# Optimization experiments

Measured on AMD Instinct MI355X. Metric: run time of the kernel, lower is better.

## Reference

```python
import jax, jax.numpy as jnp
import numpy as np

N_NODES = 50000
N_EDGES = 1_600_000
IN_DIM = 6
EMB = 64
EDGE_DIM = 1
L = 4
BN_EPS = 1e-5


def _bn_relu(x, gamma, beta):
    # BatchNorm1d in training mode: biased batch stats over the row dim.
    mu = jnp.mean(x, axis=0)
    var = jnp.var(x, axis=0)
    xhat = (x - mu) * jax.lax.rsqrt(var + BN_EPS)
    return jax.nn.relu(xhat * gamma + beta)


def setup_inputs() -> dict:
    key = jax.random.key(0)
    ks = jax.random.split(key, 32)
    s = 0.1
    inp = {
        "x": jax.random.normal(ks[0], (N_NODES, IN_DIM), jnp.float32),
        "edge_index": jax.random.randint(ks[1], (2, N_EDGES), 0, N_NODES),
        "edge_attr": jax.random.normal(ks[2], (N_EDGES, EDGE_DIM), jnp.float32),
        "lin_in_W": jax.random.normal(ks[3], (IN_DIM, EMB)) * s,
        "lin_in_b": jnp.zeros((EMB,)),
        # per-layer stacked params, leading dim L
        "msg_W1": jax.random.normal(ks[4], (L, 2 * EMB + EDGE_DIM, EMB)) * s,
        "msg_b1": jnp.zeros((L, EMB)),
        "msg_g1": jnp.ones((L, EMB)),
        "msg_be1": jnp.zeros((L, EMB)),
        "msg_W2": jax.random.normal(ks[5], (L, EMB, EMB)) * s,
        "msg_b2": jnp.zeros((L, EMB)),
        "msg_g2": jnp.ones((L, EMB)),
        "msg_be2": jnp.zeros((L, EMB)),
        "upd_W1": jax.random.normal(ks[6], (L, 2 * EMB, EMB)) * s,
        "upd_b1": jnp.zeros((L, EMB)),
        "upd_g1": jnp.ones((L, EMB)),
        "upd_be1": jnp.zeros((L, EMB)),
        "upd_W2": jax.random.normal(ks[7], (L, EMB, EMB)) * s,
        "upd_b2": jnp.zeros((L, EMB)),
        "upd_g2": jnp.ones((L, EMB)),
        "upd_be2": jnp.zeros((L, EMB)),
        "pred_W": jax.random.normal(ks[8], (EMB, 1)) * s,
        "pred_b": jnp.zeros((1,)),
    }
    return inp


def reference(x, edge_index, edge_attr, lin_in_W, lin_in_b,
              msg_W1, msg_b1, msg_g1, msg_be1, msg_W2, msg_b2, msg_g2, msg_be2,
              upd_W1, upd_b1, upd_g1, upd_be1, upd_W2, upd_b2, upd_g2, upd_be2,
              pred_W, pred_b):
    n = x.shape[0]
    src = edge_index[0]  # j (source)
    dst = edge_index[1]  # i (target / aggregation index)

    h = x @ lin_in_W + lin_in_b  # (n, d)
    for l in range(L):
        h_i = h[dst]                              # (e, d) destination feats
        h_j = h[src]                              # (e, d) source feats
        m = jnp.concatenate([h_i, h_j, edge_attr], axis=-1)  # (e, 2d+de)
        m = _bn_relu(m @ msg_W1[l] + msg_b1[l], msg_g1[l], msg_be1[l])
        m = _bn_relu(m @ msg_W2[l] + msg_b2[l], msg_g2[l], msg_be2[l])
        aggr = jax.ops.segment_sum(m, dst, num_segments=n)   # (n, d)
        u = jnp.concatenate([h, aggr], axis=-1)              # (n, 2d)
        u = _bn_relu(u @ upd_W1[l] + upd_b1[l], upd_g1[l], upd_be1[l])
        u = _bn_relu(u @ upd_W2[l] + upd_b2[l], upd_g2[l], upd_be2[l])
        h = h + u  # residual
    out = h @ pred_W + pred_b
    return out.reshape(-1)
```

## Files before the change

### kernel.cpp

```cpp
#include <hip/hip_runtime.h>
#include <hip/hip_bf16.h>


#define BN_EPS 1e-5f
#define NSH 128
#define LYS 72
#define LW1S 168
#define LW2S 68
#define ASW 66

typedef __attribute__((ext_vector_type(8))) short short8;
typedef __attribute__((ext_vector_type(16))) float floatx16;

#define MFMA32 __builtin_amdgcn_mfma_f32_32x32x16_bf16

__device__ __forceinline__ short f2bs(float f) {
  union { float f; unsigned u; } x; x.f = f;
  unsigned r = x.u + 0x7fffu + ((x.u >> 16) & 1u);
  return (short)(r >> 16);
}
__device__ __forceinline__ short f2bs_fast(float f) {
  union { float f; unsigned u; } x; x.f = f;
  return (short)((x.u + 0x8000u) >> 16);
}
__device__ __forceinline__ float bs2f(short s) {
  union { unsigned u; float f; } x;
  x.u = ((unsigned)(unsigned short)s) << 16;
  return x.f;
}


__global__ void lin_in_kernel(const float* __restrict__ x,
                              const float* __restrict__ W,
                              const float* __restrict__ b, float* __restrict__ h,
                              short* __restrict__ hb, int N) {
  int gid = blockIdx.x * blockDim.x + threadIdx.x;
  if (gid >= N * 64) return;
  int n = gid >> 6, o = gid & 63;
  float acc = b[o];
#pragma unroll
  for (int k = 0; k < 6; ++k) acc += x[n * 6 + k] * W[k * 64 + o];
  h[gid] = acc;
  hb[gid] = f2bs(acc);
}

__global__ void deg_kernel(const int* __restrict__ ei, int* __restrict__ deg,
                           int E) {
  int gid = blockIdx.x * blockDim.x + threadIdx.x;
  if (gid < E) atomicAdd(&deg[ei[E + gid]], 1);
}

__global__ void scan_kernel(const int* __restrict__ deg, int* __restrict__ offs,
                            int N) {
  __shared__ int s[1024];
  int t = threadIdx.x;
  int chunk = (N + 1023) >> 10;
  int lo = t * chunk, hi = lo + chunk;
  if (hi > N) hi = N;
  if (lo > N) lo = N;
  int tot = 0;
  for (int i = lo; i < hi; ++i) tot += deg[i];
  s[t] = tot;
  __syncthreads();
  for (int off = 1; off < 1024; off <<= 1) {
    int v = (t >= off) ? s[t - off] : 0;
    __syncthreads();
    s[t] += v;
    __syncthreads();
  }
  int run = s[t] - tot;
  for (int i = lo; i < hi; ++i) {
    offs[i] = run;
    run += deg[i];
  }
}

__global__ void fill_kernel(const int* __restrict__ ei,
                            const int* __restrict__ offs, int* __restrict__ cnt,
                            int* __restrict__ sorted, int E) {
  int gid = blockIdx.x * blockDim.x + threadIdx.x;
  if (gid >= E) return;
  int d = ei[E + gid];
  int pos = offs[d] + atomicAdd(&cnt[d], 1);
  sorted[pos] = gid;
}

__global__ void gather_edges_kernel(const int* __restrict__ ei,
                                    const int* __restrict__ sorted,
                                    const float* __restrict__ ea,
                                    int* __restrict__ dd, int* __restrict__ ds,
                                    short* __restrict__ es, int E, int Epad) {
  int i = blockIdx.x * 256 + threadIdx.x;
  if (i >= Epad) return;
  if (i < E) {
    int e = sorted[i];
    dd[i] = ei[E + e];
    ds[i] = ei[e];
    es[i] = f2bs(ea[e]);
  } else {
    dd[i] = -1;
    ds[i] = 0;
    es[i] = 0;
  }
}

__global__ void pack_w1_kernel(const float* __restrict__ W,
                               short* __restrict__ Wt, int L_) {
  int i = blockIdx.x * 256 + threadIdx.x;
  if (i >= L_ * 64 * 160) return;
  int k = i % 160, n = (i / 160) % 64, l = i / (160 * 64);
  Wt[i] = (k < 129) ? f2bs(W[((size_t)l * 129 + k) * 64 + n]) : (short)0;
}

__global__ void pack_w2_kernel(const float* __restrict__ W,
                               short* __restrict__ Wt, int L_) {
  int i = blockIdx.x * 256 + threadIdx.x;
  if (i >= L_ * 64 * 64) return;
  int k = i % 64, n = (i / 64) % 64, l = i / 4096;
  Wt[i] = f2bs(W[((size_t)l * 64 + k) * 64 + n]);
}

__global__ void bn_finalize_kernel(const float* __restrict__ shards,
                                   const float* __restrict__ gamma,
                                   const float* __restrict__ beta, float cnt,
                                   float* __restrict__ ac) {
  int o = threadIdx.x;
  float s = 0.f, q = 0.f;
  for (int i = 0; i < NSH; ++i) {
    s += shards[i * 128 + o];
    q += shards[i * 128 + 64 + o];
  }
  float mu = s / cnt;
  float var = fmaxf(q / cnt - mu * mu, 0.f);
  float r = rsqrtf(var + BN_EPS);
  float g = gamma[o];
  ac[o] = g * r;
  ac[64 + o] = beta[o] - mu * g * r;
}

__global__ void bn_finalize_pack1(const float* __restrict__ shards,
                                  const float* __restrict__ gamma,
                                  const float* __restrict__ beta, float cnt,
                                  const float* __restrict__ W,
                                  const float* __restrict__ b,
                                  short* __restrict__ Wt,
                                  float* __restrict__ bs) {
  __shared__ float sa[64];
  int t = threadIdx.x;
  if (t < 64) {
    float s = 0.f, q = 0.f;
    for (int i = 0; i < NSH; ++i) {
      s += shards[i * 128 + t];
      q += shards[i * 128 + 64 + t];
    }
    float mu = s / cnt;
    float var = fmaxf(q / cnt - mu * mu, 0.f);
    float r = rsqrtf(var + BN_EPS);
    float a = gamma[t] * r;
    float c = beta[t] - mu * a;
    sa[t] = a;
    if (blockIdx.x == 0) bs[t] = a * b[t] + c;
  }
  __syncthreads();
  int i = blockIdx.x * 256 + t;
  if (i < 64 * 160) {
    int k = i % 160, n = i / 160;
    Wt[i] = (k < 129) ? f2bs(W[k * 64 + n] * sa[n]) : (short)0;
  }
}

__global__ void bn_finalize_pack2(const float* __restrict__ shards,
                                  const float* __restrict__ gamma,
                                  const float* __restrict__ beta, float cnt,
                                  const float* __restrict__ W,
                                  const float* __restrict__ b,
                                  short* __restrict__ Wt,
                                  float* __restrict__ bs) {
  __shared__ float sa[64];
  int t = threadIdx.x;
  if (t < 64) {
    float s = 0.f, q = 0.f;
    for (int i = 0; i < NSH; ++i) {
      s += shards[i * 128 + t];
      q += shards[i * 128 + 64 + t];
    }
    float mu = s / cnt;
    float var = fmaxf(q / cnt - mu * mu, 0.f);
    float r = rsqrtf(var + BN_EPS);
    float a = gamma[t] * r;
    float c = beta[t] - mu * a;
    sa[t] = a;
    if (blockIdx.x == 0) bs[t] = a * b[t] + c;
  }
  __syncthreads();
  int i = blockIdx.x * 256 + t;
  if (i < 64 * 64) {
    int k = i % 64, n = i / 64;
    Wt[i] = f2bs(W[k * 64 + n] * sa[n]);
  }
}


__device__ __forceinline__ void stage_w1(const short* __restrict__ Wt,
                                         short* Lw, int t) {
#pragma unroll
  for (int i = 0; i < 5; ++i) {
    int c = t + i * 256;
    int col = c / 20, ch = c % 20;
    *(short8*)&Lw[col * LW1S + ch * 8] = *(const short8*)&Wt[col * 160 + ch * 8];
  }
}
__device__ __forceinline__ void stage_w2(const short* __restrict__ Wt,
                                         short* Lw, int t) {
#pragma unroll
  for (int i = 0; i < 2; ++i) {
    int c = t + i * 256;
    int col = c >> 3, ch = c & 7;
    *(short8*)&Lw[col * LW2S + ch * 8] = *(const short8*)&Wt[col * 64 + ch * 8];
  }
}

__device__ __forceinline__ void gemm1_32(const short* __restrict__ hbf,
                                         const short* Lw1,
                                         const float* __restrict__ bias, int d,
                                         int sx, short eav, int me, int hl,
                                         floatx16 acc[2]) {
  const short* hd = hbf + (size_t)d * 64 + hl * 8;
  const short* hs = hbf + (size_t)sx * 64 + hl * 8;
  short8 A[8];
#pragma unroll
  for (int kc = 0; kc < 4; ++kc) A[kc] = *(const short8*)(hd + kc * 16);
#pragma unroll
  for (int kc = 0; kc < 4; ++kc) A[4 + kc] = *(const short8*)(hs + kc * 16);
  short8 a8 = {0, 0, 0, 0, 0, 0, 0, 0};
  if (hl == 0) a8[0] = eav;
#pragma unroll
  for (int nt = 0; nt < 2; ++nt) {
    int col = nt * 32 + me;
    float bv = bias[col];
    floatx16 a;
#pragma unroll
    for (int r = 0; r < 16; ++r) a[r] = bv;
    const short* wp = Lw1 + col * LW1S + hl * 8;
#pragma unroll
    for (int kc = 0; kc < 8; ++kc) {
      short8 B = *(const short8*)(wp + kc * 16);
      a = MFMA32(A[kc], B, a, 0, 0, 0);
    }
    short8 B8 = *(const short8*)(wp + 128);
    a = MFMA32(a8, B8, a, 0, 0, 0);
    acc[nt] = a;
  }
}

__device__ __forceinline__ void gemm2_32(const short* Ly, const short* Lw2,
                                         const float* __restrict__ bias, int w,
                                         int me, int hl, floatx16 acc[2]) {
  short8 Z[4];
  const short* zp = &Ly[(w * 32 + me) * LYS + hl * 8];
#pragma unroll
  for (int kc = 0; kc < 4; ++kc) Z[kc] = *(const short8*)(zp + kc * 16);
#pragma unroll
  for (int nt = 0; nt < 2; ++nt) {
    int col = nt * 32 + me;
    float bv = bias[col];
    floatx16 a;
#pragma unroll
    for (int r = 0; r < 16; ++r) a[r] = bv;
    const short* wp = Lw2 + col * LW2S + hl * 8;
#pragma unroll
    for (int kc = 0; kc < 4; ++kc) {
      short8 B = *(const short8*)(wp + kc * 16);
      a = MFMA32(Z[kc], B, a, 0, 0, 0);
    }
    acc[nt] = a;
  }
}

__device__ __forceinline__ void stats32(const floatx16 acc[2], int idx0, int w,
                                        int hl, int lane, int E, bool full,
                                        float* sredw) {
#pragma unroll
  for (int nt = 0; nt < 2; ++nt) {
    float s = 0.f, q = 0.f;
#pragma unroll
    for (int r = 0; r < 16; ++r) {
      float v = acc[nt][r];
      if (!full) {
        int row = (r & 3) + 8 * (r >> 2) + 4 * hl;
        if (idx0 + w * 32 + row >= E) v = 0.f;
      }
      s += v;
      q += v * v;
    }
    s += __shfl_down(s, 32, 64);
    q += __shfl_down(q, 32, 64);
    if (lane < 32) {
      sredw[nt * 32 + lane] = s;
      sredw[64 + nt * 32 + lane] = q;
    }
  }
}

__device__ __forceinline__ void write_ly(short* Ly, const floatx16 acc[2],
                                         int w, int me, int hl, bool mask,
                                         int idx0, int E) {
#pragma unroll
  for (int nt = 0; nt < 2; ++nt) {
    int col = nt * 32 + me;
#pragma unroll
    for (int r = 0; r < 16; ++r) {
      int row = (r & 3) + 8 * (r >> 2) + 4 * hl;
      float v = fmaxf(acc[nt][r], 0.f);
      if (mask && idx0 + w * 32 + row >= E) v = 0.f;
      Ly[(w * 32 + row) * LYS + col] = f2bs_fast(v);
    }
  }
}


__global__ __launch_bounds__(256) void edge_pass_a(
    const short* __restrict__ hbf, const short* __restrict__ Wt1,
    const float* __restrict__ b1, const int* __restrict__ dd,
    const int* __restrict__ dsr, const short* __restrict__ es,
    float* __restrict__ stat, int E) {
  __shared__ __align__(16) short Lw1[64 * LW1S];
  __shared__ float sred[4][128];
  int t = threadIdx.x, idx0 = blockIdx.x * 128;
  stage_w1(Wt1, Lw1, t);
  __syncthreads();
  int w = t >> 6, lane = t & 63, me = lane & 31, hl = lane >> 5;
  int eg = idx0 + w * 32 + me;
  int d = dd[eg];
  int dc = d < 0 ? 0 : d;
  int sx = dsr[eg];
  short eav = es[eg];
  floatx16 acc[2];
  gemm1_32(hbf, Lw1, b1, dc, sx, eav, me, hl, acc);
  bool full = idx0 + 128 <= E;
  stats32(acc, idx0, w, hl, lane, E, full, sred[w]);
  __syncthreads();
  if (t < 128) {
    float v = sred[0][t] + sred[1][t] + sred[2][t] + sred[3][t];
    atomicAdd(&stat[(size_t)(blockIdx.x & (NSH - 1)) * 128 + t], v);
  }
}

__global__ __launch_bounds__(256) void edge_pass_b(
    const short* __restrict__ hbf, const short* __restrict__ Wt1s,
    const float* __restrict__ b1s, const int* __restrict__ dd,
    const int* __restrict__ dsr, const short* __restrict__ es,
    const short* __restrict__ Wt2, const float* __restrict__ b2,
    float* __restrict__ stat, int E) {
  __shared__ __align__(16) short Lw1[64 * LW1S];
  __shared__ __align__(16) short Lw2[64 * LW2S];
  __shared__ __align__(16) short Ly[128 * LYS];
  __shared__ float sred[4][128];
  int t = threadIdx.x, idx0 = blockIdx.x * 128;
  stage_w1(Wt1s, Lw1, t);
  stage_w2(Wt2, Lw2, t);
  __syncthreads();
  int w = t >> 6, lane = t & 63, me = lane & 31, hl = lane >> 5;
  int eg = idx0 + w * 32 + me;
  int d = dd[eg];
  int dc = d < 0 ? 0 : d;
  int sx = dsr[eg];
  short eav = es[eg];
  floatx16 acc[2];
  gemm1_32(hbf, Lw1, b1s, dc, sx, eav, me, hl, acc);
  write_ly(Ly, acc, w, me, hl, false, idx0, E);
  floatx16 acc2[2];
  gemm2_32(Ly, Lw2, b2, w, me, hl, acc2);
  bool full = idx0 + 128 <= E;
  stats32(acc2, idx0, w, hl, lane, E, full, sred[w]);
  __syncthreads();
  if (t < 128) {
    float v = sred[0][t] + sred[1][t] + sred[2][t] + sred[3][t];
    atomicAdd(&stat[(size_t)(blockIdx.x & (NSH - 1)) * 128 + t], v);
  }
}

__global__ __launch_bounds__(256) void edge_pass_c(
    const short* __restrict__ hbf, const short* __restrict__ Wt1s,
    const float* __restrict__ b1s, const int* __restrict__ dd,
    const int* __restrict__ dsr, const short* __restrict__ es,
    const short* __restrict__ Wt2s, const float* __restrict__ b2s,
    float* __restrict__ aggr, int E) {
  __shared__ __align__(16) short Lw1[64 * LW1S];
  __shared__ __align__(16) short Lw2[64 * LW2S];
  __shared__ __align__(16) short Ly[128 * LYS];
  __shared__ int sdst[128];
  int t = threadIdx.x, idx0 = blockIdx.x * 128;
  if (t < 128) sdst[t] = dd[idx0 + t];
  stage_w1(Wt1s, Lw1, t);
  stage_w2(Wt2s, Lw2, t);
  __syncthreads();
  int w = t >> 6, lane = t & 63, me = lane & 31, hl = lane >> 5;
  int eg = idx0 + w * 32 + me;
  int d = sdst[w * 32 + me];
  int dc = d < 0 ? 0 : d;
  int sx = dsr[eg];
  short eav = es[eg];
  floatx16 acc[2];
  gemm1_32(hbf, Lw1, b1s, dc, sx, eav, me, hl, acc);
  write_ly(Ly, acc, w, me, hl, false, idx0, E);
  floatx16 acc2[2];
  gemm2_32(Ly, Lw2, b2s, w, me, hl, acc2);
  bool full = idx0 + 128 <= E;
  write_ly(Ly, acc2, w, me, hl, !full, idx0, E);
  __syncthreads();
  int scol = t & 63, g = t >> 6;
  float s = 0.f;
  int e0 = g * 32;
  for (int e = e0; e < e0 + 32; ++e) {
    int d2 = sdst[e];
    s += bs2f(Ly[e * LYS + scol]);
    int dn = (e == e0 + 31) ? -2 : sdst[e + 1];
    if (d2 != dn) {
      if (d2 >= 0) atomicAdd(&aggr[(size_t)d2 * 64 + scol], s);
      s = 0.f;
    }
  }
}


__device__ __forceinline__ void gemm_r2c8(const float* __restrict__ As,
                                          const float* __restrict__ W, int K,
                                          int rg, int cg, float acc[2][8]) {
  const float* ap = As + rg * 2;
  const float* wp = W + cg * 8;
#pragma unroll 4
  for (int k = 0; k < K; ++k) {
    float2 a = *(const float2*)&ap[k * ASW];
    float4 w0 = *(const float4*)&wp[k * 64];
    float4 w1 = *(const float4*)&wp[k * 64 + 4];
    float wv[8] = {w0.x, w0.y, w0.z, w0.w, w1.x, w1.y, w1.z, w1.w};
#pragma unroll
    for (int j = 0; j < 8; ++j) {
      acc[0][j] += a.x * wv[j];
      acc[1][j] += a.y * wv[j];
    }
  }
}

__device__ __forceinline__ void stats_r2c8(const float acc[2][8],
                                           float* __restrict__ shard, int t,
                                           int cg) {
  float s[8], q[8];
#pragma unroll
  for (int j = 0; j < 8; ++j) {
    s[j] = acc[0][j] + acc[1][j];
    q[j] = acc[0][j] * acc[0][j] + acc[1][j] * acc[1][j];
  }
#pragma unroll
  for (int off = 32; off >= 8; off >>= 1) {
#pragma unroll
    for (int j = 0; j < 8; ++j) {
      s[j] += __shfl_down(s[j], off, 64);
      q[j] += __shfl_down(q[j], off, 64);
    }
  }
  if (((t & 63) >> 3) == 0) {
#pragma unroll
    for (int j = 0; j < 8; ++j) {
      atomicAdd(&shard[cg * 8 + j], s[j]);
      atomicAdd(&shard[64 + cg * 8 + j], q[j]);
    }
  }
}

__global__ __launch_bounds__(256) void node_gemm1_v3(
    const float* __restrict__ h, const float* __restrict__ aggr,
    const float* __restrict__ W, const float* __restrict__ b,
    float* __restrict__ u1, float* __restrict__ stat, int N) {
  __shared__ __align__(16) float As[128 * ASW];
  int n0 = blockIdx.x * 64;
  int t = threadIdx.x;
  int c = t & 63, g = t >> 6;
  for (int n = g; n < 64; n += 4) {
    int idx = n0 + n;
    bool v = idx < N;
    As[c * ASW + n] = v ? h[(size_t)idx * 64 + c] : 0.f;
    As[(64 + c) * ASW + n] = v ? aggr[(size_t)idx * 64 + c] : 0.f;
  }
  __syncthreads();
  int rg = t >> 3, cg = t & 7;
  float acc[2][8];
#pragma unroll
  for (int i = 0; i < 2; ++i)
#pragma unroll
    for (int j = 0; j < 8; ++j) acc[i][j] = b[cg * 8 + j];
  gemm_r2c8(As, W, 128, rg, cg, acc);
#pragma unroll
  for (int i = 0; i < 2; ++i) {
    int idx = n0 + rg * 2 + i;
    if (idx < N) {
      *(float4*)&u1[(size_t)idx * 64 + cg * 8] =
          make_float4(acc[i][0], acc[i][1], acc[i][2], acc[i][3]);
      *(float4*)&u1[(size_t)idx * 64 + cg * 8 + 4] =
          make_float4(acc[i][4], acc[i][5], acc[i][6], acc[i][7]);
    } else {
#pragma unroll
      for (int j = 0; j < 8; ++j) acc[i][j] = 0.f;
    }
  }
  stats_r2c8(acc, stat + (size_t)(blockIdx.x & (NSH - 1)) * 128, t, cg);
}

__global__ __launch_bounds__(256) void node_gemm2_v3(
    const float* __restrict__ u1, const float* __restrict__ ac,
    const float* __restrict__ W, const float* __restrict__ b,
    float* __restrict__ u2, float* __restrict__ stat, int N) {
  __shared__ __align__(16) float As[64 * ASW];
  int n0 = blockIdx.x * 64;
  int t = threadIdx.x;
  int c = t & 63, g = t >> 6;
  float a1 = ac[c], c1 = ac[64 + c];
  for (int n = g; n < 64; n += 4) {
    int idx = n0 + n;
    bool v = idx < N;
    As[c * ASW + n] = v ? fmaxf(u1[(size_t)idx * 64 + c] * a1 + c1, 0.f) : 0.f;
  }
  __syncthreads();
  int rg = t >> 3, cg = t & 7;
  float acc[2][8];
#pragma unroll
  for (int i = 0; i < 2; ++i)
#pragma unroll
    for (int j = 0; j < 8; ++j) acc[i][j] = b[cg * 8 + j];
  gemm_r2c8(As, W, 64, rg, cg, acc);
#pragma unroll
  for (int i = 0; i < 2; ++i) {
    int idx = n0 + rg * 2 + i;
    if (idx < N) {
      *(float4*)&u2[(size_t)idx * 64 + cg * 8] =
          make_float4(acc[i][0], acc[i][1], acc[i][2], acc[i][3]);
      *(float4*)&u2[(size_t)idx * 64 + cg * 8 + 4] =
          make_float4(acc[i][4], acc[i][5], acc[i][6], acc[i][7]);
    } else {
#pragma unroll
      for (int j = 0; j < 8; ++j) acc[i][j] = 0.f;
    }
  }
  stats_r2c8(acc, stat + (size_t)(blockIdx.x & (NSH - 1)) * 128, t, cg);
}

__global__ void residual_kernel(float* __restrict__ h, short* __restrict__ hb,
                                const float* __restrict__ u2,
                                const float* __restrict__ ac, int total) {
  int gid = blockIdx.x * blockDim.x + threadIdx.x;
  if (gid >= total) return;
  int o = gid & 63;
  float v = u2[gid] * ac[o] + ac[64 + o];
  float nv = h[gid] + fmaxf(v, 0.f);
  h[gid] = nv;
  hb[gid] = f2bs(nv);
}

__global__ void pred_kernel(const float* __restrict__ h,
                            const float* __restrict__ W,
                            const float* __restrict__ b,
                            float* __restrict__ out, int N) {
  int n = blockIdx.x * blockDim.x + threadIdx.x;
  if (n >= N) return;
  float acc = b[0];
  const float* hr = h + (size_t)n * 64;
#pragma unroll
  for (int o = 0; o < 64; ++o) acc += hr[o] * W[o];
  out[n] = acc;
}


extern "C" void kernel_launch(void* const* d_in, const int* in_sizes, int n_in,
                              void* d_out, int out_size, void* d_ws,
                              size_t ws_size, hipStream_t stream) {
  const float* x = (const float*)d_in[0];
  const int* ei = (const int*)d_in[1];
  const float* ea = (const float*)d_in[2];
  const float* lin_W = (const float*)d_in[3];
  const float* lin_b = (const float*)d_in[4];
  const float* msg_W1 = (const float*)d_in[5];
  const float* msg_b1 = (const float*)d_in[6];
  const float* msg_g1 = (const float*)d_in[7];
  const float* msg_be1 = (const float*)d_in[8];
  const float* msg_W2 = (const float*)d_in[9];
  const float* msg_b2 = (const float*)d_in[10];
  const float* msg_g2 = (const float*)d_in[11];
  const float* msg_be2 = (const float*)d_in[12];
  const float* upd_W1 = (const float*)d_in[13];
  const float* upd_b1 = (const float*)d_in[14];
  const float* upd_g1 = (const float*)d_in[15];
  const float* upd_be1 = (const float*)d_in[16];
  const float* upd_W2 = (const float*)d_in[17];
  const float* upd_b2 = (const float*)d_in[18];
  const float* upd_g2 = (const float*)d_in[19];
  const float* upd_be2 = (const float*)d_in[20];
  const float* pred_W = (const float*)d_in[21];
  const float* pred_b = (const float*)d_in[22];
  float* out = (float*)d_out;

  const int N = in_sizes[0] / 6;
  const int E = in_sizes[1] / 2;
  const int L = 4;
  const int Epad = ((E + 127) / 128) * 128;

  char* p = (char*)d_ws;
  auto alloc = [&](size_t bytes) {
    void* r = (void*)p;
    p += (bytes + 255) & ~(size_t)255;
    return r;
  };
  float* h = (float*)alloc((size_t)N * 64 * 4);
  short* hb = (short*)alloc((size_t)N * 64 * 2);
  float* aggr = (float*)alloc((size_t)N * 64 * 4);
  float* u1 = (float*)alloc((size_t)N * 64 * 4);
  float* u2 = (float*)alloc((size_t)N * 64 * 4);
  float* stats = (float*)alloc((size_t)4 * NSH * 128 * 4);
  float* acu1 = (float*)alloc(128 * 4);
  float* acu2 = (float*)alloc(128 * 4);
  float* b1s = (float*)alloc(64 * 4);
  float* b2s = (float*)alloc(64 * 4);
  int* deg = (int*)alloc((size_t)N * 4);
  int* offs = (int*)alloc((size_t)N * 4);
  int* cnt = (int*)alloc((size_t)N * 4);
  int* sorted = (int*)alloc((size_t)E * 4);
  int* dd = (int*)alloc((size_t)Epad * 4);
  int* dsr = (int*)alloc((size_t)Epad * 4);
  short* es = (short*)alloc((size_t)Epad * 2);
  short* Wt1 = (short*)alloc((size_t)L * 64 * 160 * 2);
  short* Wt2 = (short*)alloc((size_t)L * 64 * 64 * 2);
  short* Wt1s = (short*)alloc((size_t)64 * 160 * 2);
  short* Wt2s = (short*)alloc((size_t)64 * 64 * 2);

  const int B = 256;
  const size_t REG = (size_t)NSH * 128;
  int gridE256 = (E + 255) / 256;
  int gridEb = Epad / 128;
  int gridM64 = (N + 63) / 64;
  int gridN64 = (N * 64 + B - 1) / B;
  int gridN = (N + B - 1) / B;

  hipMemsetAsync(deg, 0, (size_t)N * 4, stream);
  hipMemsetAsync(cnt, 0, (size_t)N * 4, stream);
  lin_in_kernel<<<gridN64, B, 0, stream>>>(x, lin_W, lin_b, h, hb, N);
  deg_kernel<<<gridE256, B, 0, stream>>>(ei, deg, E);
  scan_kernel<<<1, 1024, 0, stream>>>(deg, offs, N);
  fill_kernel<<<gridE256, B, 0, stream>>>(ei, offs, cnt, sorted, E);
  gather_edges_kernel<<<(Epad + 255) / 256, B, 0, stream>>>(ei, sorted, ea, dd,
                                                            dsr, es, E, Epad);
  pack_w1_kernel<<<(L * 64 * 160 + 255) / 256, B, 0, stream>>>(msg_W1, Wt1, L);
  pack_w2_kernel<<<(L * 64 * 64 + 255) / 256, B, 0, stream>>>(msg_W2, Wt2, L);

  for (int l = 0; l < L; ++l) {
    const short* Wt1l = Wt1 + (size_t)l * 64 * 160;
    const short* Wt2l = Wt2 + (size_t)l * 64 * 64;
    const float* U1 = upd_W1 + (size_t)l * 128 * 64;
    const float* U2 = upd_W2 + (size_t)l * 64 * 64;
    hipMemsetAsync(stats, 0, (size_t)4 * REG * 4, stream);
    hipMemsetAsync(aggr, 0, (size_t)N * 64 * 4, stream);
    edge_pass_a<<<gridEb, 256, 0, stream>>>(hb, Wt1l, msg_b1 + l * 64, dd, dsr,
                                            es, stats, E);
    bn_finalize_pack1<<<(64 * 160 + 255) / 256, B, 0, stream>>>(
        stats, msg_g1 + l * 64, msg_be1 + l * 64, (float)E,
        msg_W1 + (size_t)l * 129 * 64, msg_b1 + l * 64, Wt1s, b1s);
    edge_pass_b<<<gridEb, 256, 0, stream>>>(hb, Wt1s, b1s, dd, dsr, es, Wt2l,
                                            msg_b2 + l * 64, stats + REG, E);
    bn_finalize_pack2<<<(64 * 64 + 255) / 256, B, 0, stream>>>(
        stats + REG, msg_g2 + l * 64, msg_be2 + l * 64, (float)E,
        msg_W2 + (size_t)l * 64 * 64, msg_b2 + l * 64, Wt2s, b2s);
    edge_pass_c<<<gridEb, 256, 0, stream>>>(hb, Wt1s, b1s, dd, dsr, es, Wt2s,
                                            b2s, aggr, E);
    node_gemm1_v3<<<gridM64, 256, 0, stream>>>(h, aggr, U1, upd_b1 + l * 64,
                                               u1, stats + 2 * REG, N);
    bn_finalize_kernel<<<1, 64, 0, stream>>>(stats + 2 * REG, upd_g1 + l * 64,
                                             upd_be1 + l * 64, (float)N, acu1);
    node_gemm2_v3<<<gridM64, 256, 0, stream>>>(u1, acu1, U2, upd_b2 + l * 64,
                                               u2, stats + 3 * REG, N);
    bn_finalize_kernel<<<1, 64, 0, stream>>>(stats + 3 * REG, upd_g2 + l * 64,
                                             upd_be2 + l * 64, (float)N, acu2);
    residual_kernel<<<gridN64, B, 0, stream>>>(h, hb, u2, acu2, N * 64);
  }
  pred_kernel<<<gridN, B, 0, stream>>>(h, pred_W, pred_b, out, N);
}
```

Measured before the change: 2.082 ms.

## Cache pre-BN edge activations in workspace instead of recomputing edge GEMMs

Pass A now writes the raw first-layer message GEMM output to a bf16 workspace buffer, and pass B reads it back, applies the BN affine and ReLU, and runs only the second GEMM. Pass B also stores its raw output so pass C only needs the BN affine, ReLU and segment-sum, with no GEMMs. This removes the recomputed gathers and MFMA work in passes B and C. In exchange it adds large global reads and writes, and edges beyond the workspace capacity fall back to recomputation. It also loops several tiles per block, stores node intermediates u1/u2 as bf16, and merges the two memsets into one.

New measurement: 2.420 ms. 1.16x slower.

```diff
diff --git a/kernel.cpp b/kernel.cpp
--- a/kernel.cpp
+++ b/kernel.cpp
@@ -4,6 +4,7 @@
 
 #define BN_EPS 1e-5f
 #define NSH 128
+#define TPB 4
 #define LYS 72
 #define LW1S 168
 #define LW2S 68
@@ -143,8 +144,8 @@
                                   const float* __restrict__ beta, float cnt,
                                   const float* __restrict__ W,
                                   const float* __restrict__ b,
-                                  short* __restrict__ Wt,
-                                  float* __restrict__ bs) {
+                                  short* __restrict__ Wt, float* __restrict__ bs,
+                                  float* __restrict__ ac) {
   __shared__ float sa[64];
   int t = threadIdx.x;
   if (t < 64) {
@@ -159,7 +160,11 @@
     float a = gamma[t] * r;
     float c = beta[t] - mu * a;
     sa[t] = a;
-    if (blockIdx.x == 0) bs[t] = a * b[t] + c;
+    if (blockIdx.x == 0) {
+      bs[t] = a * b[t] + c;
+      ac[t] = a;
+      ac[64 + t] = c;
+    }
   }
   __syncthreads();
   int i = blockIdx.x * 256 + t;
@@ -174,8 +179,8 @@
                                   const float* __restrict__ beta, float cnt,
                                   const float* __restrict__ W,
                                   const float* __restrict__ b,
-                                  short* __restrict__ Wt,
-                                  float* __restrict__ bs) {
+                                  short* __restrict__ Wt, float* __restrict__ bs,
+                                  float* __restrict__ ac) {
   __shared__ float sa[64];
   int t = threadIdx.x;
   if (t < 64) {
@@ -190,7 +195,11 @@
     float a = gamma[t] * r;
     float c = beta[t] - mu * a;
     sa[t] = a;
-    if (blockIdx.x == 0) bs[t] = a * b[t] + c;
+    if (blockIdx.x == 0) {
+      bs[t] = a * b[t] + c;
+      ac[t] = a;
+      ac[64 + t] = c;
+    }
   }
   __syncthreads();
   int i = blockIdx.x * 256 + t;
@@ -253,13 +262,16 @@
   }
 }
 
-__device__ __forceinline__ void gemm2_32(const short* Ly, const short* Lw2,
-                                         const float* __restrict__ bias, int w,
-                                         int me, int hl, floatx16 acc[2]) {
-  short8 Z[4];
+__device__ __forceinline__ void load_z_ly(const short* Ly, int w, int me,
+                                          int hl, short8 Z[4]) {
   const short* zp = &Ly[(w * 32 + me) * LYS + hl * 8];
 #pragma unroll
   for (int kc = 0; kc < 4; ++kc) Z[kc] = *(const short8*)(zp + kc * 16);
+}
+
+__device__ __forceinline__ void gemm2_core(const short8 Z[4], const short* Lw2,
+                                           const float* __restrict__ bias,
+                                           int me, int hl, floatx16 acc[2]) {
 #pragma unroll
   for (int nt = 0; nt < 2; ++nt) {
     int col = nt * 32 + me;
@@ -277,9 +289,9 @@
   }
 }
 
-__device__ __forceinline__ void stats32(const floatx16 acc[2], int idx0, int w,
-                                        int hl, int lane, int E, bool full,
-                                        float* sredw) {
+__device__ __forceinline__ void stats32_acc(const floatx16 acc[2], int idx0,
+                                            int w, int hl, int E, bool full,
+                                            float sa[2], float qa[2]) {
 #pragma unroll
   for (int nt = 0; nt < 2; ++nt) {
     float s = 0.f, q = 0.f;
@@ -295,10 +307,8 @@
     }
     s += __shfl_down(s, 32, 64);
     q += __shfl_down(q, 32, 64);
-    if (lane < 32) {
-      sredw[nt * 32 + lane] = s;
-      sredw[64 + nt * 32 + lane] = q;
-    }
+    sa[nt] += s;
+    qa[nt] += q;
   }
 }
 
@@ -318,27 +328,70 @@
   }
 }
 
+__device__ __forceinline__ void write_ly_raw(short* Ly, const floatx16 acc[2],
+                                             int w, int me, int hl) {
+#pragma unroll
+  for (int nt = 0; nt < 2; ++nt) {
+    int col = nt * 32 + me;
+#pragma unroll
+    for (int r = 0; r < 16; ++r) {
+      int row = (r & 3) + 8 * (r >> 2) + 4 * hl;
+      Ly[(w * 32 + row) * LYS + col] = f2bs_fast(acc[nt][r]);
+    }
+  }
+}
+
+__device__ __forceinline__ void ly_to_g(const short* Ly, short* y, int t) {
+#pragma unroll
+  for (int i = 0; i < 4; ++i) {
+    int c = t + i * 256;
+    int row = c >> 3, ch = c & 7;
+    *(short8*)&y[(size_t)row * 64 + ch * 8] =
+        *(const short8*)&Ly[row * LYS + ch * 8];
+  }
+}
+
 
 __global__ __launch_bounds__(256) void edge_pass_a(
     const short* __restrict__ hbf, const short* __restrict__ Wt1,
     const float* __restrict__ b1, const int* __restrict__ dd,
     const int* __restrict__ dsr, const short* __restrict__ es,
-    float* __restrict__ stat, int E) {
+    float* __restrict__ stat, short* __restrict__ ybuf, int E, int Epad,
+    int Ecap) {
   __shared__ __align__(16) short Lw1[64 * LW1S];
+  __shared__ __align__(16) short Ly[128 * LYS];
   __shared__ float sred[4][128];
-  int t = threadIdx.x, idx0 = blockIdx.x * 128;
+  int t = threadIdx.x;
   stage_w1(Wt1, Lw1, t);
   __syncthreads();
   int w = t >> 6, lane = t & 63, me = lane & 31, hl = lane >> 5;
-  int eg = idx0 + w * 32 + me;
-  int d = dd[eg];
-  int dc = d < 0 ? 0 : d;
-  int sx = dsr[eg];
-  short eav = es[eg];
-  floatx16 acc[2];
-  gemm1_32(hbf, Lw1, b1, dc, sx, eav, me, hl, acc);
-  bool full = idx0 + 128 <= E;
-  stats32(acc, idx0, w, hl, lane, E, full, sred[w]);
+  float sa[2] = {0.f, 0.f}, qa[2] = {0.f, 0.f};
+  for (int it = 0; it < TPB; ++it) {
+    int idx0 = (blockIdx.x * TPB + it) * 128;
+    if (idx0 >= Epad) break;
+    int eg = idx0 + w * 32 + me;
+    int d = dd[eg];
+    int dc = d < 0 ? 0 : d;
+    int sx = dsr[eg];
+    short eav = es[eg];
+    floatx16 acc[2];
+    gemm1_32(hbf, Lw1, b1, dc, sx, eav, me, hl, acc);
+    bool full = idx0 + 128 <= E;
+    stats32_acc(acc, idx0, w, hl, E, full, sa, qa);
+    if (idx0 < Ecap) {
+      write_ly_raw(Ly, acc, w, me, hl);
+      __syncthreads();
+      ly_to_g(Ly, ybuf + (size_t)idx0 * 64, t);
+      __syncthreads();
+    }
+  }
+  if (lane < 32) {
+#pragma unroll
+    for (int nt = 0; nt < 2; ++nt) {
+      sred[w][nt * 32 + lane] = sa[nt];
+      sred[w][64 + nt * 32 + lane] = qa[nt];
+    }
+  }
   __syncthreads();
   if (t < 128) {
     float v = sred[0][t] + sred[1][t] + sred[2][t] + sred[3][t];
@@ -348,31 +401,73 @@
 
 __global__ __launch_bounds__(256) void edge_pass_b(
     const short* __restrict__ hbf, const short* __restrict__ Wt1s,
-    const float* __restrict__ b1s, const int* __restrict__ dd,
-    const int* __restrict__ dsr, const short* __restrict__ es,
-    const short* __restrict__ Wt2, const float* __restrict__ b2,
-    float* __restrict__ stat, int E) {
+    const float* __restrict__ b1s, const float* __restrict__ ac1,
+    const int* __restrict__ dd, const int* __restrict__ dsr,
+    const short* __restrict__ es, const short* __restrict__ Wt2,
+    const float* __restrict__ b2, float* __restrict__ stat,
+    short* __restrict__ ybuf, int E, int Epad, int Ecap) {
   __shared__ __align__(16) short Lw1[64 * LW1S];
   __shared__ __align__(16) short Lw2[64 * LW2S];
   __shared__ __align__(16) short Ly[128 * LYS];
   __shared__ float sred[4][128];
-  int t = threadIdx.x, idx0 = blockIdx.x * 128;
-  stage_w1(Wt1s, Lw1, t);
+  int t = threadIdx.x;
+  bool anyrec = ((blockIdx.x * TPB + TPB - 1) * 128) >= Ecap;
+  if (anyrec) stage_w1(Wt1s, Lw1, t);
   stage_w2(Wt2, Lw2, t);
   __syncthreads();
   int w = t >> 6, lane = t & 63, me = lane & 31, hl = lane >> 5;
-  int eg = idx0 + w * 32 + me;
-  int d = dd[eg];
-  int dc = d < 0 ? 0 : d;
-  int sx = dsr[eg];
-  short eav = es[eg];
-  floatx16 acc[2];
-  gemm1_32(hbf, Lw1, b1s, dc, sx, eav, me, hl, acc);
-  write_ly(Ly, acc, w, me, hl, false, idx0, E);
-  floatx16 acc2[2];
-  gemm2_32(Ly, Lw2, b2, w, me, hl, acc2);
-  bool full = idx0 + 128 <= E;
-  stats32(acc2, idx0, w, hl, lane, E, full, sred[w]);
+  float sa[2] = {0.f, 0.f}, qa[2] = {0.f, 0.f};
+  for (int it = 0; it < TPB; ++it) {
+    int idx0 = (blockIdx.x * TPB + it) * 128;
+    if (idx0 >= Epad) break;
+    bool full = idx0 + 128 <= E;
+    floatx16 acc2[2];
+    if (idx0 < Ecap) {
+      const short* yp = ybuf + (size_t)(idx0 + w * 32 + me) * 64 + hl * 8;
+      short8 Z[4];
+#pragma unroll
+      for (int kc = 0; kc < 4; ++kc) {
+        short8 Y = *(const short8*)(yp + kc * 16);
+        int k0 = kc * 16 + hl * 8;
+        float4 a0 = *(const float4*)&ac1[k0];
+        float4 a1 = *(const float4*)&ac1[k0 + 4];
+        float4 c0 = *(const float4*)&ac1[64 + k0];
+        float4 c1 = *(const float4*)&ac1[64 + k0 + 4];
+        float av[8] = {a0.x, a0.y, a0.z, a0.w, a1.x, a1.y, a1.z, a1.w};
+        float cv[8] = {c0.x, c0.y, c0.z, c0.w, c1.x, c1.y, c1.z, c1.w};
+        short8 z;
+#pragma unroll
+        for (int j = 0; j < 8; ++j)
+          z[j] = f2bs_fast(fmaxf(bs2f(Y[j]) * av[j] + cv[j], 0.f));
+        Z[kc] = z;
+      }
+      gemm2_core(Z, Lw2, b2, me, hl, acc2);
+      write_ly_raw(Ly, acc2, w, me, hl);
+      __syncthreads();
+      ly_to_g(Ly, ybuf + (size_t)idx0 * 64, t);
+      __syncthreads();
+    } else {
+      int eg = idx0 + w * 32 + me;
+      int d = dd[eg];
+      int dc = d < 0 ? 0 : d;
+      int sx = dsr[eg];
+      short eav = es[eg];
+      floatx16 acc[2];
+      gemm1_32(hbf, Lw1, b1s, dc, sx, eav, me, hl, acc);
+      write_ly(Ly, acc, w, me, hl, false, idx0, E);
+      short8 Z[4];
+      load_z_ly(Ly, w, me, hl, Z);
+      gemm2_core(Z, Lw2, b2, me, hl, acc2);
+    }
+    stats32_acc(acc2, idx0, w, hl, E, full, sa, qa);
+  }
+  if (lane < 32) {
+#pragma unroll
+    for (int nt = 0; nt < 2; ++nt) {
+      sred[w][nt * 32 + lane] = sa[nt];
+      sred[w][64 + nt * 32 + lane] = qa[nt];
+    }
+  }
   __syncthreads();
   if (t < 128) {
     float v = sred[0][t] + sred[1][t] + sred[2][t] + sred[3][t];
@@ -385,41 +480,69 @@
     const float* __restrict__ b1s, const int* __restrict__ dd,
     const int* __restrict__ dsr, const short* __restrict__ es,
     const short* __restrict__ Wt2s, const float* __restrict__ b2s,
-    float* __restrict__ aggr, int E) {
+    const float* __restrict__ ac2, float* __restrict__ aggr,
+    const short* __restrict__ ybuf, int E, int Epad, int Ecap) {
   __shared__ __align__(16) short Lw1[64 * LW1S];
   __shared__ __align__(16) short Lw2[64 * LW2S];
   __shared__ __align__(16) short Ly[128 * LYS];
   __shared__ int sdst[128];
-  int t = threadIdx.x, idx0 = blockIdx.x * 128;
-  if (t < 128) sdst[t] = dd[idx0 + t];
-  stage_w1(Wt1s, Lw1, t);
-  stage_w2(Wt2s, Lw2, t);
+  int t = threadIdx.x;
+  bool anyrec = ((blockIdx.x * TPB + TPB - 1) * 128) >= Ecap;
+  if (anyrec) {
+    stage_w1(Wt1s, Lw1, t);
+    stage_w2(Wt2s, Lw2, t);
+  }
   __syncthreads();
   int w = t >> 6, lane = t & 63, me = lane & 31, hl = lane >> 5;
-  int eg = idx0 + w * 32 + me;
-  int d = sdst[w * 32 + me];
-  int dc = d < 0 ? 0 : d;
-  int sx = dsr[eg];
-  short eav = es[eg];
-  floatx16 acc[2];
-  gemm1_32(hbf, Lw1, b1s, dc, sx, eav, me, hl, acc);
-  write_ly(Ly, acc, w, me, hl, false, idx0, E);
-  floatx16 acc2[2];
-  gemm2_32(Ly, Lw2, b2s, w, me, hl, acc2);
-  bool full = idx0 + 128 <= E;
-  write_ly(Ly, acc2, w, me, hl, !full, idx0, E);
-  __syncthreads();
   int scol = t & 63, g = t >> 6;
-  float s = 0.f;
-  int e0 = g * 32;
-  for (int e = e0; e < e0 + 32; ++e) {
-    int d2 = sdst[e];
-    s += bs2f(Ly[e * LYS + scol]);
-    int dn = (e == e0 + 31) ? -2 : sdst[e + 1];
-    if (d2 != dn) {
-      if (d2 >= 0) atomicAdd(&aggr[(size_t)d2 * 64 + scol], s);
-      s = 0.f;
-    }
+  for (int it = 0; it < TPB; ++it) {
+    int idx0 = (blockIdx.x * TPB + it) * 128;
+    if (idx0 >= Epad) break;
+    if (t < 128) sdst[t] = dd[idx0 + t];
+    __syncthreads();
+    if (idx0 < Ecap) {
+      float a2 = ac2[scol], c2 = ac2[64 + scol];
+      const short* yrow = ybuf + (size_t)idx0 * 64 + scol;
+      float s = 0.f;
+      int e0 = g * 32;
+      for (int e = e0; e < e0 + 32; ++e) {
+        int d2 = sdst[e];
+        s += fmaxf(bs2f(yrow[(size_t)e * 64]) * a2 + c2, 0.f);
+        int dn = (e == e0 + 31) ? -2 : sdst[e + 1];
+        if (d2 != dn) {
+          if (d2 >= 0) atomicAdd(&aggr[(size_t)d2 * 64 + scol], s);
+          s = 0.f;
+        }
+      }
+    } else {
+      int eg = idx0 + w * 32 + me;
+      int d = sdst[w * 32 + me];
+      int dc = d < 0 ? 0 : d;
+      int sx = dsr[eg];
+      short eav = es[eg];
+      floatx16 acc[2];
+      gemm1_32(hbf, Lw1, b1s, dc, sx, eav, me, hl, acc);
+      write_ly(Ly, acc, w, me, hl, false, idx0, E);
+      short8 Z[4];
+      load_z_ly(Ly, w, me, hl, Z);
+      floatx16 acc2[2];
+      gemm2_core(Z, Lw2, b2s, me, hl, acc2);
+      bool full = idx0 + 128 <= E;
+      write_ly(Ly, acc2, w, me, hl, !full, idx0, E);
+      __syncthreads();
+      float s = 0.f;
+      int e0 = g * 32;
+      for (int e = e0; e < e0 + 32; ++e) {
+        int d2 = sdst[e];
+        s += bs2f(Ly[e * LYS + scol]);
+        int dn = (e == e0 + 31) ? -2 : sdst[e + 1];
+        if (d2 != dn) {
+          if (d2 >= 0) atomicAdd(&aggr[(size_t)d2 * 64 + scol], s);
+          s = 0.f;
+        }
+      }
+    }
+    __syncthreads();
   }
 }
 
@@ -472,7 +595,7 @@
 __global__ __launch_bounds__(256) void node_gemm1_v3(
     const float* __restrict__ h, const float* __restrict__ aggr,
     const float* __restrict__ W, const float* __restrict__ b,
-    float* __restrict__ u1, float* __restrict__ stat, int N) {
+    short* __restrict__ u1, float* __restrict__ stat, int N) {
   __shared__ __align__(16) float As[128 * ASW];
   int n0 = blockIdx.x * 64;
   int t = threadIdx.x;
@@ -495,10 +618,10 @@
   for (int i = 0; i < 2; ++i) {
     int idx = n0 + rg * 2 + i;
     if (idx < N) {
-      *(float4*)&u1[(size_t)idx * 64 + cg * 8] =
-          make_float4(acc[i][0], acc[i][1], acc[i][2], acc[i][3]);
-      *(float4*)&u1[(size_t)idx * 64 + cg * 8 + 4] =
-          make_float4(acc[i][4], acc[i][5], acc[i][6], acc[i][7]);
+      short8 o;
+#pragma unroll
+      for (int j = 0; j < 8; ++j) o[j] = f2bs(acc[i][j]);
+      *(short8*)&u1[(size_t)idx * 64 + cg * 8] = o;
     } else {
 #pragma unroll
       for (int j = 0; j < 8; ++j) acc[i][j] = 0.f;
@@ -508,9 +631,9 @@
 }
 
 __global__ __launch_bounds__(256) void node_gemm2_v3(
-    const float* __restrict__ u1, const float* __restrict__ ac,
+    const short* __restrict__ u1, const float* __restrict__ ac,
     const float* __restrict__ W, const float* __restrict__ b,
-    float* __restrict__ u2, float* __restrict__ stat, int N) {
+    short* __restrict__ u2, float* __restrict__ stat, int N) {
   __shared__ __align__(16) float As[64 * ASW];
   int n0 = blockIdx.x * 64;
   int t = threadIdx.x;
@@ -519,7 +642,8 @@
   for (int n = g; n < 64; n += 4) {
     int idx = n0 + n;
     bool v = idx < N;
-    As[c * ASW + n] = v ? fmaxf(u1[(size_t)idx * 64 + c] * a1 + c1, 0.f) : 0.f;
+    As[c * ASW + n] =
+        v ? fmaxf(bs2f(u1[(size_t)idx * 64 + c]) * a1 + c1, 0.f) : 0.f;
   }
   __syncthreads();
   int rg = t >> 3, cg = t & 7;
@@ -533,10 +657,10 @@
   for (int i = 0; i < 2; ++i) {
     int idx = n0 + rg * 2 + i;
     if (idx < N) {
-      *(float4*)&u2[(size_t)idx * 64 + cg * 8] =
-          make_float4(acc[i][0], acc[i][1], acc[i][2], acc[i][3]);
-      *(float4*)&u2[(size_t)idx * 64 + cg * 8 + 4] =
-          make_float4(acc[i][4], acc[i][5], acc[i][6], acc[i][7]);
+      short8 o;
+#pragma unroll
+      for (int j = 0; j < 8; ++j) o[j] = f2bs(acc[i][j]);
+      *(short8*)&u2[(size_t)idx * 64 + cg * 8] = o;
     } else {
 #pragma unroll
       for (int j = 0; j < 8; ++j) acc[i][j] = 0.f;
@@ -546,12 +670,12 @@
 }
 
 __global__ void residual_kernel(float* __restrict__ h, short* __restrict__ hb,
-                                const float* __restrict__ u2,
+                                const short* __restrict__ u2,
                                 const float* __restrict__ ac, int total) {
   int gid = blockIdx.x * blockDim.x + threadIdx.x;
   if (gid >= total) return;
   int o = gid & 63;
-  float v = u2[gid] * ac[o] + ac[64 + o];
+  float v = bs2f(u2[gid]) * ac[o] + ac[64 + o];
   float nv = h[gid] + fmaxf(v, 0.f);
   h[gid] = nv;
   hb[gid] = f2bs(nv);
@@ -613,17 +737,15 @@
   float* h = (float*)alloc((size_t)N * 64 * 4);
   short* hb = (short*)alloc((size_t)N * 64 * 2);
   float* aggr = (float*)alloc((size_t)N * 64 * 4);
-  float* u1 = (float*)alloc((size_t)N * 64 * 4);
-  float* u2 = (float*)alloc((size_t)N * 64 * 4);
   float* stats = (float*)alloc((size_t)4 * NSH * 128 * 4);
+  float* ac1 = (float*)alloc(128 * 4);
+  float* ac2 = (float*)alloc(128 * 4);
   float* acu1 = (float*)alloc(128 * 4);
   float* acu2 = (float*)alloc(128 * 4);
   float* b1s = (float*)alloc(64 * 4);
   float* b2s = (float*)alloc(64 * 4);
-  int* deg = (int*)alloc((size_t)N * 4);
-  int* offs = (int*)alloc((size_t)N * 4);
-  int* cnt = (int*)alloc((size_t)N * 4);
-  int* sorted = (int*)alloc((size_t)E * 4);
+  short* u1 = (short*)alloc((size_t)N * 64 * 2);
+  short* u2 = (short*)alloc((size_t)N * 64 * 2);
   int* dd = (int*)alloc((size_t)Epad * 4);
   int* dsr = (int*)alloc((size_t)Epad * 4);
   short* es = (short*)alloc((size_t)Epad * 2);
@@ -631,11 +753,24 @@
   short* Wt2 = (short*)alloc((size_t)L * 64 * 64 * 2);
   short* Wt1s = (short*)alloc((size_t)64 * 160 * 2);
   short* Wt2s = (short*)alloc((size_t)64 * 64 * 2);
+  char* pS = p;
+  int* deg = (int*)alloc((size_t)N * 4);
+  int* offs = (int*)alloc((size_t)N * 4);
+  int* cnt = (int*)alloc((size_t)N * 4);
+  int* sorted = (int*)alloc((size_t)E * 4);
+  short* ybuf = (short*)pS;
+  size_t remaining =
+      (ws_size > (size_t)(pS - (char*)d_ws)) ? ws_size - (size_t)(pS - (char*)d_ws) : 0;
+  long long ecap_e = (long long)(remaining / 128);
+  long long ecap_t = (ecap_e / 128) * 128;
+  int Ecap = (ecap_t > (long long)Epad) ? Epad : (int)ecap_t;
+  if (Ecap < 0) Ecap = 0;
 
   const int B = 256;
   const size_t REG = (size_t)NSH * 128;
   int gridE256 = (E + 255) / 256;
-  int gridEb = Epad / 128;
+  int NT = Epad / 128;
+  int gridEdge = (NT + TPB - 1) / TPB;
   int gridM64 = (N + 63) / 64;
   int gridN64 = (N * 64 + B - 1) / B;
   int gridN = (N + B - 1) / B;
@@ -656,20 +791,22 @@
     const short* Wt2l = Wt2 + (size_t)l * 64 * 64;
     const float* U1 = upd_W1 + (size_t)l * 128 * 64;
     const float* U2 = upd_W2 + (size_t)l * 64 * 64;
-    hipMemsetAsync(stats, 0, (size_t)4 * REG * 4, stream);
-    hipMemsetAsync(aggr, 0, (size_t)N * 64 * 4, stream);
-    edge_pass_a<<<gridEb, 256, 0, stream>>>(hb, Wt1l, msg_b1 + l * 64, dd, dsr,
-                                            es, stats, E);
+    hipMemsetAsync(aggr, 0, (size_t)N * 64 * 4 + (size_t)4 * REG * 4, stream);
+    edge_pass_a<<<gridEdge, 256, 0, stream>>>(hb, Wt1l, msg_b1 + l * 64, dd,
+                                              dsr, es, stats, ybuf, E, Epad,
+                                              Ecap);
     bn_finalize_pack1<<<(64 * 160 + 255) / 256, B, 0, stream>>>(
         stats, msg_g1 + l * 64, msg_be1 + l * 64, (float)E,
-        msg_W1 + (size_t)l * 129 * 64, msg_b1 + l * 64, Wt1s, b1s);
-    edge_pass_b<<<gridEb, 256, 0, stream>>>(hb, Wt1s, b1s, dd, dsr, es, Wt2l,
-                                            msg_b2 + l * 64, stats + REG, E);
+        msg_W1 + (size_t)l * 129 * 64, msg_b1 + l * 64, Wt1s, b1s, ac1);
+    edge_pass_b<<<gridEdge, 256, 0, stream>>>(
+        hb, Wt1s, b1s, ac1, dd, dsr, es, Wt2l, msg_b2 + l * 64, stats + REG,
+        ybuf, E, Epad, Ecap);
     bn_finalize_pack2<<<(64 * 64 + 255) / 256, B, 0, stream>>>(
         stats + REG, msg_g2 + l * 64, msg_be2 + l * 64, (float)E,
-        msg_W2 + (size_t)l * 64 * 64, msg_b2 + l * 64, Wt2s, b2s);
-    edge_pass_c<<<gridEb, 256, 0, stream>>>(hb, Wt1s, b1s, dd, dsr, es, Wt2s,
-                                            b2s, aggr, E);
+        msg_W2 + (size_t)l * 64 * 64, msg_b2 + l * 64, Wt2s, b2s, ac2);
+    edge_pass_c<<<gridEdge, 256, 0, stream>>>(hb, Wt1s, b1s, dd, dsr, es, Wt2s,
+                                              b2s, ac2, aggr, ybuf, E, Epad,
+                                              Ecap);
     node_gemm1_v3<<<gridM64, 256, 0, stream>>>(h, aggr, U1, upd_b1 + l * 64,
                                                u1, stats + 2 * REG, N);
     bn_finalize_kernel<<<1, 64, 0, stream>>>(stats + 2 * REG, upd_g1 + l * 64,
```
